# Performance work log

Hardware: AMD Instinct MI355X
Metric: run time of the kernel (lower is better)

The kernel has to match this reference:

```python
import jax, jax.numpy as jnp
import numpy as np

EPS = 1e-5

def layer_norm(x, g, b):
    m = x.mean(-1, keepdims=True)
    v = ((x - m) ** 2).mean(-1, keepdims=True)
    return (x - m) * jax.lax.rsqrt(v + EPS) * g + b

def setup_inputs() -> dict:
    key = jax.random.key(0)
    ks = jax.random.split(key, 12)
    H = 2048; E = 2048; I = 2048; N = 32
    A = (H + E) // 2  # attention hidden = 2048
    s = lambda fan: 1.0 / np.sqrt(fan)
    inp = {
        "input":   jax.random.normal(ks[0], (I,), jnp.float32),
        "hiddens": jax.random.normal(ks[1], (N, H), jnp.float32),
        "cells":   jax.random.normal(ks[2], (N, H), jnp.float32),
        "external":jax.random.normal(ks[3], (E,), jnp.float32),
        # weights (torch nn.Linear layout: [out, in]); LN enabled -> no biases on linears
        "W_ai":   jax.random.uniform(ks[4], (A, H + E), jnp.float32, -s(H+E), s(H+E)),
        "W_attn": jax.random.uniform(ks[5], (1, A), jnp.float32, -s(A), s(A)),
        "W_merge":jax.random.uniform(ks[6], (H, H), jnp.float32, -s(H), s(H)),
        "W_iou":  jax.random.uniform(ks[7], (3 * H, I + H), jnp.float32, -s(I+H), s(I+H)),
        "W_fi":   jax.random.uniform(ks[8], (H, I), jnp.float32, -s(I), s(I)),
        "W_fh":   jax.random.uniform(ks[9], (H, H), jnp.float32, -s(H), s(H)),
        "g_merge": jnp.ones((H,), jnp.float32), "b_merge": jnp.zeros((H,), jnp.float32),
        "g_f": jnp.ones((H,), jnp.float32), "b_f": jnp.zeros((H,), jnp.float32),
        "g_i": jnp.ones((H,), jnp.float32), "b_i": jnp.zeros((H,), jnp.float32),
        "g_o": jnp.ones((H,), jnp.float32), "b_o": jnp.zeros((H,), jnp.float32),
        "g_u": jnp.ones((H,), jnp.float32), "b_u": jnp.zeros((H,), jnp.float32),
        "g_c": jnp.ones((H,), jnp.float32), "b_c": jnp.zeros((H,), jnp.float32),
    }
    return inp

def reference(input, hiddens, cells, external,
              W_ai, W_attn, W_merge, W_iou, W_fi, W_fh,
              g_merge, b_merge, g_f, b_f, g_i, b_i, g_o, b_o, g_u, b_u, g_c, b_c):
    N, H = hiddens.shape
    # forget-gate preactivations: [H] + [N,H] -> [N,H]
    f_lin = input @ W_fi.T + hiddens @ W_fh.T
    # attentive merge over children
    ext = jnp.broadcast_to(external, (N, external.shape[0]))
    ai = jnp.tanh(jnp.concatenate([hiddens, ext], axis=1) @ W_ai.T)       # [N, (H+E)//2]
    attn = jax.nn.softmax(ai @ W_attn.T, axis=0)                          # [N, 1]
    merged = (hiddens * attn).sum(0)                                      # [H]
    merge_hidden = jnp.tanh(layer_norm(merged @ W_merge.T, g_merge, b_merge))
    # i/o/u gates from [input ; merged_hidden]
    iou = jnp.concatenate([input, merge_hidden]) @ W_iou.T                # [3H]
    i_l, o_l, u_l = jnp.split(iou, 3)
    f = jax.nn.sigmoid(layer_norm(f_lin, g_f, b_f))                       # [N,H]
    i = jax.nn.sigmoid(layer_norm(i_l, g_i, b_i))
    o = jax.nn.sigmoid(layer_norm(o_l, g_o, b_o))
    u = jnp.tanh(layer_norm(u_l, g_u, b_u))                               # dropout=0 -> identity
    new_cell = layer_norm(i * u + (f * cells).sum(0), g_c, b_c)           # [H]
    new_h = o * jnp.tanh(new_cell)
    return new_h, new_cell
```

## Files before the change

### kernel.cpp

```cpp
#include <hip/hip_runtime.h>
#include <hip/hip_bf16.h>

typedef __bf16 bf16_t;
typedef __attribute__((ext_vector_type(8))) __bf16 bf16x8;
typedef __attribute__((ext_vector_type(4))) float f32x4;

#define EPSF 1e-5f

__global__ __launch_bounds__(256, 3) void k1_streams(
    const float* __restrict__ hiddens, const float* __restrict__ external,
    const float* __restrict__ input,
    const float* __restrict__ W_ai, const float* __restrict__ W_fh,
    const float* __restrict__ W_fi, const float* __restrict__ W_iou,
    const float* __restrict__ W_attn,
    float* __restrict__ lp, float* __restrict__ fh_out,
    float* __restrict__ fi_out, float* __restrict__ iou_out)
{
    __shared__ float red[4][2][16][16];
    __shared__ float ejs[4][16];

    int b    = blockIdx.x;
    int tid  = threadIdx.x;
    int wave = tid >> 6;
    int lane = tid & 63;

    if (b < 256) {
        bool is_ai = (b < 128);
        int  jt    = is_ai ? b : b - 128;
        int  l15   = lane & 15;
        int  quad  = lane >> 4;
        int  k0    = wave * 512;
        int  wstride = is_ai ? 4096 : 2048;
        const float* W = is_ai ? W_ai : W_fh;

        const float* a0p = hiddens + (size_t)l15 * 2048 + quad * 8 + k0;
        const float* a1p = hiddens + (size_t)(16 + l15) * 2048 + quad * 8 + k0;
        const float* bp  = W + (size_t)(jt * 16 + l15) * wstride + quad * 8 + k0;

        f32x4 acc0 = {0.f, 0.f, 0.f, 0.f};
        f32x4 acc1 = {0.f, 0.f, 0.f, 0.f};
        float ejacc = 0.f;

        if (is_ai) {
            const float* ep = bp + 2048;
            const float* xp = external + quad * 8 + k0;
            #pragma unroll 2
            for (int k = 0; k < 512; k += 32) {
                float4 p0 = *(const float4*)(a0p + k);
                float4 p1 = *(const float4*)(a0p + k + 4);
                float4 q0 = *(const float4*)(a1p + k);
                float4 q1 = *(const float4*)(a1p + k + 4);
                float4 b0 = *(const float4*)(bp + k);
                float4 b1 = *(const float4*)(bp + k + 4);
                float4 e0 = *(const float4*)(ep + k);
                float4 e1 = *(const float4*)(ep + k + 4);
                float4 x0 = *(const float4*)(xp + k);
                float4 x1 = *(const float4*)(xp + k + 4);
                bf16x8 av0, av1, bv;
                av0[0]=(bf16_t)p0.x; av0[1]=(bf16_t)p0.y; av0[2]=(bf16_t)p0.z; av0[3]=(bf16_t)p0.w;
                av0[4]=(bf16_t)p1.x; av0[5]=(bf16_t)p1.y; av0[6]=(bf16_t)p1.z; av0[7]=(bf16_t)p1.w;
                av1[0]=(bf16_t)q0.x; av1[1]=(bf16_t)q0.y; av1[2]=(bf16_t)q0.z; av1[3]=(bf16_t)q0.w;
                av1[4]=(bf16_t)q1.x; av1[5]=(bf16_t)q1.y; av1[6]=(bf16_t)q1.z; av1[7]=(bf16_t)q1.w;
                bv[0]=(bf16_t)b0.x; bv[1]=(bf16_t)b0.y; bv[2]=(bf16_t)b0.z; bv[3]=(bf16_t)b0.w;
                bv[4]=(bf16_t)b1.x; bv[5]=(bf16_t)b1.y; bv[6]=(bf16_t)b1.z; bv[7]=(bf16_t)b1.w;
                acc0 = __builtin_amdgcn_mfma_f32_16x16x32_bf16(av0, bv, acc0, 0, 0, 0);
                acc1 = __builtin_amdgcn_mfma_f32_16x16x32_bf16(av1, bv, acc1, 0, 0, 0);
                ejacc += e0.x*x0.x + e0.y*x0.y + e0.z*x0.z + e0.w*x0.w
                       + e1.x*x1.x + e1.y*x1.y + e1.z*x1.z + e1.w*x1.w;
            }
            ejacc += __shfl_xor(ejacc, 16, 64);
            ejacc += __shfl_xor(ejacc, 32, 64);
            if (quad == 0) ejs[wave][l15] = ejacc;
        } else {
            #pragma unroll 2
            for (int k = 0; k < 512; k += 32) {
                float4 p0 = *(const float4*)(a0p + k);
                float4 p1 = *(const float4*)(a0p + k + 4);
                float4 q0 = *(const float4*)(a1p + k);
                float4 q1 = *(const float4*)(a1p + k + 4);
                float4 b0 = *(const float4*)(bp + k);
                float4 b1 = *(const float4*)(bp + k + 4);
                bf16x8 av0, av1, bv;
                av0[0]=(bf16_t)p0.x; av0[1]=(bf16_t)p0.y; av0[2]=(bf16_t)p0.z; av0[3]=(bf16_t)p0.w;
                av0[4]=(bf16_t)p1.x; av0[5]=(bf16_t)p1.y; av0[6]=(bf16_t)p1.z; av0[7]=(bf16_t)p1.w;
                av1[0]=(bf16_t)q0.x; av1[1]=(bf16_t)q0.y; av1[2]=(bf16_t)q0.z; av1[3]=(bf16_t)q0.w;
                av1[4]=(bf16_t)q1.x; av1[5]=(bf16_t)q1.y; av1[6]=(bf16_t)q1.z; av1[7]=(bf16_t)q1.w;
                bv[0]=(bf16_t)b0.x; bv[1]=(bf16_t)b0.y; bv[2]=(bf16_t)b0.z; bv[3]=(bf16_t)b0.w;
                bv[4]=(bf16_t)b1.x; bv[5]=(bf16_t)b1.y; bv[6]=(bf16_t)b1.z; bv[7]=(bf16_t)b1.w;
                acc0 = __builtin_amdgcn_mfma_f32_16x16x32_bf16(av0, bv, acc0, 0, 0, 0);
                acc1 = __builtin_amdgcn_mfma_f32_16x16x32_bf16(av1, bv, acc1, 0, 0, 0);
            }
        }

        #pragma unroll
        for (int r = 0; r < 4; ++r) {
            red[wave][0][quad * 4 + r][l15] = acc0[r];
            red[wave][1][quad * 4 + r][l15] = acc1[r];
        }
        __syncthreads();

        int row = tid >> 4, col = tid & 15;
        #pragma unroll
        for (int nt = 0; nt < 2; ++nt) {
            float s = red[0][nt][row][col] + red[1][nt][row][col]
                    + red[2][nt][row][col] + red[3][nt][row][col];
            if (is_ai) {
                float ej = ejs[0][col] + ejs[1][col] + ejs[2][col] + ejs[3][col];
                float lg = tanhf(s + ej) * W_attn[jt * 16 + col];
                lg += __shfl_xor(lg, 1, 64);
                lg += __shfl_xor(lg, 2, 64);
                lg += __shfl_xor(lg, 4, 64);
                lg += __shfl_xor(lg, 8, 64);
                if (col == 0) lp[jt * 32 + nt * 16 + row] = lg;
            } else {
                fh_out[(size_t)(nt * 16 + row) * 2048 + jt * 16 + col] = s;
            }
        }
    } else {
        const float4* in4 = (const float4*)input;
        float4 xr[8];
        #pragma unroll
        for (int k = 0; k < 8; ++k) xr[k] = in4[lane + 64 * k];

        int r0 = (b - 256) * 16 + wave * 4;
        #pragma unroll
        for (int p = 0; p < 2; ++p) {
            int ra = r0 + p * 2;
            int rb = ra + 1;
            const float4* wa = (ra < 2048)
                ? (const float4*)(W_fi + (size_t)ra * 2048)
                : (const float4*)(W_iou + (size_t)(ra - 2048) * 4096);
            const float4* wb = (rb < 2048)
                ? (const float4*)(W_fi + (size_t)rb * 2048)
                : (const float4*)(W_iou + (size_t)(rb - 2048) * 4096);
            float4 A[8], B[8];
            #pragma unroll
            for (int k = 0; k < 8; ++k) { A[k] = wa[lane + 64 * k]; B[k] = wb[lane + 64 * k]; }
            float accA = 0.f, accB = 0.f;
            #pragma unroll
            for (int k = 0; k < 8; ++k) {
                accA += A[k].x*xr[k].x + A[k].y*xr[k].y + A[k].z*xr[k].z + A[k].w*xr[k].w;
                accB += B[k].x*xr[k].x + B[k].y*xr[k].y + B[k].z*xr[k].z + B[k].w*xr[k].w;
            }
            #pragma unroll
            for (int off = 32; off; off >>= 1) {
                accA += __shfl_down(accA, off, 64);
                accB += __shfl_down(accB, off, 64);
            }
            if (lane == 0) {
                if (ra < 2048) fi_out[ra] = accA; else iou_out[ra - 2048] = accA;
                if (rb < 2048) fi_out[rb] = accB; else iou_out[rb - 2048] = accB;
            }
        }
    }
}

__global__ __launch_bounds__(256) void k2_mid(
    const float* __restrict__ fi, const float* __restrict__ fh,
    const float* __restrict__ lp, const float* __restrict__ hiddens,
    float* __restrict__ frs, float* __restrict__ merged)
{
    __shared__ float s1[256], s2[256];
    int b = blockIdx.x, t = threadIdx.x;

    if (b < 32) {
        int n = b;
        float sum = 0.f, sq = 0.f;
        #pragma unroll
        for (int i = 0; i < 8; ++i) {
            int h = t * 8 + i;
            float v = fi[h] + fh[n * 2048 + h];
            sum += v; sq += v * v;
        }
        s1[t] = sum; s2[t] = sq;
        __syncthreads();
        for (int off = 128; off; off >>= 1) {
            if (t < off) { s1[t] += s1[t + off]; s2[t] += s2[t + off]; }
            __syncthreads();
        }
        if (t == 0) {
            const float inv = 1.f / 2048.f;
            float mean = s1[0] * inv;
            frs[n * 2]     = mean;
            frs[n * 2 + 1] = rsqrtf(s2[0] * inv - mean * mean + EPSF);
        }
    } else {
        __shared__ float lred[32][8];
        __shared__ float attnw[32];
        int n = t >> 3, sl = t & 7;
        float p = 0.f;
        #pragma unroll
        for (int m = 0; m < 16; ++m) p += lp[(sl * 16 + m) * 32 + n];
        lred[n][sl] = p;
        __syncthreads();
        if (sl == 0) {
            float lg = 0.f;
            #pragma unroll
            for (int m = 0; m < 8; ++m) lg += lred[n][m];
            lred[n][0] = lg;
        }
        __syncthreads();
        if (t < 32) {
            float mx = -1e30f;
            for (int m = 0; m < 32; ++m) mx = fmaxf(mx, lred[m][0]);
            float ssum = 0.f;
            for (int m = 0; m < 32; ++m) ssum += expf(lred[m][0] - mx);
            attnw[t] = expf(lred[t][0] - mx) / ssum;
        }
        __syncthreads();
        int h = (b - 32) * 256 + t;
        float acc = 0.f;
        #pragma unroll 8
        for (int n2 = 0; n2 < 32; ++n2) acc += attnw[n2] * hiddens[n2 * 2048 + h];
        merged[h] = acc;
    }
}

__global__ __launch_bounds__(256) void k3_mid(
    const float* __restrict__ W_merge, const float* __restrict__ merged,
    const float* __restrict__ fi, const float* __restrict__ fh,
    const float* __restrict__ frs, const float* __restrict__ gf,
    const float* __restrict__ bf_, const float* __restrict__ cells,
    float* __restrict__ mm, float* __restrict__ fc)
{
    int b = blockIdx.x, t = threadIdx.x;
    int wave = t >> 6, lane = t & 63;
    if (b < 256) {
        const float4* xp = (const float4*)merged;
        float4 xr[8];
        #pragma unroll
        for (int k = 0; k < 8; ++k) xr[k] = xp[lane + 64 * k];

        int ra = b * 8 + wave * 2;
        int rb = ra + 1;
        const float4* wa = (const float4*)(W_merge + (size_t)ra * 2048);
        const float4* wb = (const float4*)(W_merge + (size_t)rb * 2048);
        float4 A[8], B[8];
        #pragma unroll
        for (int k = 0; k < 8; ++k) { A[k] = wa[lane + 64 * k]; B[k] = wb[lane + 64 * k]; }
        float accA = 0.f, accB = 0.f;
        #pragma unroll
        for (int k = 0; k < 8; ++k) {
            accA += A[k].x*xr[k].x + A[k].y*xr[k].y + A[k].z*xr[k].z + A[k].w*xr[k].w;
            accB += B[k].x*xr[k].x + B[k].y*xr[k].y + B[k].z*xr[k].z + B[k].w*xr[k].w;
        }
        #pragma unroll
        for (int off = 32; off; off >>= 1) {
            accA += __shfl_down(accA, off, 64);
            accB += __shfl_down(accB, off, 64);
        }
        if (lane == 0) { mm[ra] = accA; mm[rb] = accB; }
    } else {
        int h = (b - 256) * 256 + t;
        float g = gf[h], bb = bf_[h], f_i = fi[h];
        float acc = 0.f;
        #pragma unroll 8
        for (int n = 0; n < 32; ++n) {
            float v = (f_i + fh[n * 2048 + h] - frs[n * 2]) * frs[n * 2 + 1] * g + bb;
            float f = 1.f / (1.f + expf(-v));
            acc += f * cells[n * 2048 + h];
        }
        fc[h] = acc;
    }
}

__global__ __launch_bounds__(256, 3) void k4_mh(
    const float* __restrict__ W_iou, const float* __restrict__ mm,
    const float* __restrict__ g_merge, const float* __restrict__ b_merge,
    float* __restrict__ iou)
{
    __shared__ float mh_lds[2048];
    __shared__ float pr[4][2];
    int b = blockIdx.x, t = threadIdx.x;
    int wave = t >> 6, lane = t & 63;

    const float4* mm4 = (const float4*)mm;
    const float4* g4  = (const float4*)g_merge;
    const float4* b4  = (const float4*)b_merge;

    float4 m0 = mm4[t * 2], m1 = mm4[t * 2 + 1];
    float sum = m0.x + m0.y + m0.z + m0.w + m1.x + m1.y + m1.z + m1.w;
    float sq  = m0.x*m0.x + m0.y*m0.y + m0.z*m0.z + m0.w*m0.w
              + m1.x*m1.x + m1.y*m1.y + m1.z*m1.z + m1.w*m1.w;
    #pragma unroll
    for (int off = 1; off < 64; off <<= 1) {
        sum += __shfl_xor(sum, off, 64);
        sq  += __shfl_xor(sq,  off, 64);
    }
    if (lane == 0) { pr[wave][0] = sum; pr[wave][1] = sq; }
    __syncthreads();
    sum = pr[0][0] + pr[1][0] + pr[2][0] + pr[3][0];
    sq  = pr[0][1] + pr[1][1] + pr[2][1] + pr[3][1];
    const float inv = 1.f / 2048.f;
    float mean = sum * inv;
    float r = rsqrtf(sq * inv - mean * mean + EPSF);

    float4 g0 = g4[t * 2], g1 = g4[t * 2 + 1];
    float4 c0 = b4[t * 2], c1 = b4[t * 2 + 1];
    float4 h0, h1;
    h0.x = tanhf((m0.x - mean) * r * g0.x + c0.x);
    h0.y = tanhf((m0.y - mean) * r * g0.y + c0.y);
    h0.z = tanhf((m0.z - mean) * r * g0.z + c0.z);
    h0.w = tanhf((m0.w - mean) * r * g0.w + c0.w);
    h1.x = tanhf((m1.x - mean) * r * g1.x + c1.x);
    h1.y = tanhf((m1.y - mean) * r * g1.y + c1.y);
    h1.z = tanhf((m1.z - mean) * r * g1.z + c1.z);
    h1.w = tanhf((m1.w - mean) * r * g1.w + c1.w);
    ((float4*)mh_lds)[t * 2]     = h0;
    ((float4*)mh_lds)[t * 2 + 1] = h1;
    __syncthreads();

    float4 xr[8];
    #pragma unroll
    for (int k = 0; k < 8; ++k) xr[k] = ((const float4*)mh_lds)[lane + 64 * k];

    int ra = b * 8 + wave * 2;
    int rb = ra + 1;
    const float4* wa = (const float4*)(W_iou + (size_t)ra * 4096 + 2048);
    const float4* wb = (const float4*)(W_iou + (size_t)rb * 4096 + 2048);
    float4 A[8], B[8];
    #pragma unroll
    for (int k = 0; k < 8; ++k) { A[k] = wa[lane + 64 * k]; B[k] = wb[lane + 64 * k]; }
    float accA = 0.f, accB = 0.f;
    #pragma unroll
    for (int k = 0; k < 8; ++k) {
        accA += A[k].x*xr[k].x + A[k].y*xr[k].y + A[k].z*xr[k].z + A[k].w*xr[k].w;
        accB += B[k].x*xr[k].x + B[k].y*xr[k].y + B[k].z*xr[k].z + B[k].w*xr[k].w;
    }
    #pragma unroll
    for (int off = 32; off; off >>= 1) {
        accA += __shfl_down(accA, off, 64);
        accB += __shfl_down(accB, off, 64);
    }
    if (lane == 0) { iou[ra] += accA; iou[rb] += accB; }
}

__global__ __launch_bounds__(256) void k5_tail(
    const float* __restrict__ iou, const float* __restrict__ fc,
    const float* __restrict__ gi, const float* __restrict__ bi,
    const float* __restrict__ go, const float* __restrict__ bo,
    const float* __restrict__ gu, const float* __restrict__ bu,
    const float* __restrict__ gc, const float* __restrict__ bc,
    float* __restrict__ out)
{
    __shared__ float sA[6][256];
    int t = threadIdx.x;
    float vi[8], vo[8], vu[8];
    float si = 0, qi = 0, so = 0, qo = 0, su = 0, qu = 0;
    #pragma unroll
    for (int i = 0; i < 8; ++i) {
        int h = t * 8 + i;
        vi[i] = iou[h]; vo[i] = iou[2048 + h]; vu[i] = iou[4096 + h];
        si += vi[i]; qi += vi[i] * vi[i];
        so += vo[i]; qo += vo[i] * vo[i];
        su += vu[i]; qu += vu[i] * vu[i];
    }
    sA[0][t] = si; sA[1][t] = qi; sA[2][t] = so;
    sA[3][t] = qo; sA[4][t] = su; sA[5][t] = qu;
    __syncthreads();
    for (int off = 128; off; off >>= 1) {
        if (t < off) {
            #pragma unroll
            for (int c = 0; c < 6; ++c) sA[c][t] += sA[c][t + off];
        }
        __syncthreads();
    }
    const float inv = 1.f / 2048.f;
    float mi = sA[0][0] * inv, ri = rsqrtf(sA[1][0] * inv - mi * mi + EPSF);
    float mo = sA[2][0] * inv, ro = rsqrtf(sA[3][0] * inv - mo * mo + EPSF);
    float mu = sA[4][0] * inv, ru = rsqrtf(sA[5][0] * inv - mu * mu + EPSF);
    __syncthreads();

    float o_[8], v_[8];
    float sv = 0, qv = 0;
    #pragma unroll
    for (int i = 0; i < 8; ++i) {
        int h = t * 8 + i;
        float ivl = 1.f / (1.f + expf(-((vi[i] - mi) * ri * gi[h] + bi[h])));
        o_[i]     = 1.f / (1.f + expf(-((vo[i] - mo) * ro * go[h] + bo[h])));
        float uvl = tanhf((vu[i] - mu) * ru * gu[h] + bu[h]);
        v_[i] = ivl * uvl + fc[h];
        sv += v_[i]; qv += v_[i] * v_[i];
    }
    sA[0][t] = sv; sA[1][t] = qv;
    __syncthreads();
    for (int off = 128; off; off >>= 1) {
        if (t < off) { sA[0][t] += sA[0][t + off]; sA[1][t] += sA[1][t + off]; }
        __syncthreads();
    }
    float mc = sA[0][0] * inv, rc = rsqrtf(sA[1][0] * inv - mc * mc + EPSF);
    #pragma unroll
    for (int i = 0; i < 8; ++i) {
        int h = t * 8 + i;
        float nc = (v_[i] - mc) * rc * gc[h] + bc[h];
        float nh = o_[i] * tanhf(nc);
        out[h]        = nh;
        out[2048 + h] = nc;
    }
}

extern "C" void kernel_launch(void* const* d_in, const int* in_sizes, int n_in,
                              void* d_out, int out_size, void* d_ws, size_t ws_size,
                              hipStream_t stream)
{
    const float* input    = (const float*)d_in[0];
    const float* hiddens  = (const float*)d_in[1];
    const float* cells    = (const float*)d_in[2];
    const float* external = (const float*)d_in[3];
    const float* W_ai     = (const float*)d_in[4];
    const float* W_attn   = (const float*)d_in[5];
    const float* W_merge  = (const float*)d_in[6];
    const float* W_iou    = (const float*)d_in[7];
    const float* W_fi     = (const float*)d_in[8];
    const float* W_fh     = (const float*)d_in[9];
    const float* g_merge  = (const float*)d_in[10];
    const float* b_merge  = (const float*)d_in[11];
    const float* g_f      = (const float*)d_in[12];
    const float* b_f      = (const float*)d_in[13];
    const float* g_i      = (const float*)d_in[14];
    const float* b_i      = (const float*)d_in[15];
    const float* g_o      = (const float*)d_in[16];
    const float* b_o      = (const float*)d_in[17];
    const float* g_u      = (const float*)d_in[18];
    const float* b_u      = (const float*)d_in[19];
    const float* g_c      = (const float*)d_in[20];
    const float* b_c      = (const float*)d_in[21];

    float* ws = (float*)d_ws;
    float* ws_fh     = ws;
    float* ws_fi     = ws + 65536;
    float* ws_lp     = ws + 67584;
    float* ws_frs    = ws + 71680;
    float* ws_merged = ws + 71744;
    float* ws_mm     = ws + 73792;
    float* ws_fc     = ws + 75840;
    float* ws_iou    = ws + 77888;
    float* out = (float*)d_out;

    k1_streams<<<768, 256, 0, stream>>>(hiddens, external, input,
                                        W_ai, W_fh, W_fi, W_iou, W_attn,
                                        ws_lp, ws_fh, ws_fi, ws_iou);
    k2_mid<<<40, 256, 0, stream>>>(ws_fi, ws_fh, ws_lp, hiddens,
                                   ws_frs, ws_merged);
    k3_mid<<<264, 256, 0, stream>>>(W_merge, ws_merged, ws_fi, ws_fh,
                                    ws_frs, g_f, b_f, cells, ws_mm, ws_fc);
    k4_mh<<<768, 256, 0, stream>>>(W_iou, ws_mm, g_merge, b_merge, ws_iou);
    k5_tail<<<1, 256, 0, stream>>>(ws_iou, ws_fc, g_i, b_i, g_o, b_o,
                                   g_u, b_u, g_c, b_c, out);
}
```

Baseline: 278.5 us.

## Move input half of W_iou GEMV from k1 into k4 full-row pass

The input-side half of the W_iou matvec moves out of the first streaming kernel into the merge-hidden kernel, so k4 reads full 4096-wide W_iou rows once and writes iou directly instead of read-modify-write. k1 shrinks to 512 blocks (W_fi only), and k4 uses 256 blocks with 6 rows per wave and double-buffered register row loads. This shortens k1 but puts more weight streaming after the serial dependency chain (k2/k3), where it can no longer overlap with other independent work. Register pressure rises sharply in k4 (launch bounds set to 1 block/CU).

```diff
diff --git a/kernel.cpp b/kernel.cpp
--- a/kernel.cpp
+++ b/kernel.cpp
@@ -7,14 +7,13 @@
 
 #define EPSF 1e-5f
 
-__global__ __launch_bounds__(256, 3) void k1_streams(
+__global__ __launch_bounds__(256, 2) void k1_streams(
     const float* __restrict__ hiddens, const float* __restrict__ external,
     const float* __restrict__ input,
     const float* __restrict__ W_ai, const float* __restrict__ W_fh,
-    const float* __restrict__ W_fi, const float* __restrict__ W_iou,
-    const float* __restrict__ W_attn,
+    const float* __restrict__ W_fi, const float* __restrict__ W_attn,
     float* __restrict__ lp, float* __restrict__ fh_out,
-    float* __restrict__ fi_out, float* __restrict__ iou_out)
+    float* __restrict__ fi_out)
 {
     __shared__ float red[4][2][16][16];
     __shared__ float ejs[4][16];
@@ -122,36 +121,25 @@
         #pragma unroll
         for (int k = 0; k < 8; ++k) xr[k] = in4[lane + 64 * k];
 
-        int r0 = (b - 256) * 16 + wave * 4;
-        #pragma unroll
-        for (int p = 0; p < 2; ++p) {
-            int ra = r0 + p * 2;
-            int rb = ra + 1;
-            const float4* wa = (ra < 2048)
-                ? (const float4*)(W_fi + (size_t)ra * 2048)
-                : (const float4*)(W_iou + (size_t)(ra - 2048) * 4096);
-            const float4* wb = (rb < 2048)
-                ? (const float4*)(W_fi + (size_t)rb * 2048)
-                : (const float4*)(W_iou + (size_t)(rb - 2048) * 4096);
-            float4 A[8], B[8];
-            #pragma unroll
-            for (int k = 0; k < 8; ++k) { A[k] = wa[lane + 64 * k]; B[k] = wb[lane + 64 * k]; }
-            float accA = 0.f, accB = 0.f;
-            #pragma unroll
-            for (int k = 0; k < 8; ++k) {
-                accA += A[k].x*xr[k].x + A[k].y*xr[k].y + A[k].z*xr[k].z + A[k].w*xr[k].w;
-                accB += B[k].x*xr[k].x + B[k].y*xr[k].y + B[k].z*xr[k].z + B[k].w*xr[k].w;
-            }
-            #pragma unroll
-            for (int off = 32; off; off >>= 1) {
-                accA += __shfl_down(accA, off, 64);
-                accB += __shfl_down(accB, off, 64);
-            }
-            if (lane == 0) {
-                if (ra < 2048) fi_out[ra] = accA; else iou_out[ra - 2048] = accA;
-                if (rb < 2048) fi_out[rb] = accB; else iou_out[rb - 2048] = accB;
-            }
-        }
+        int ra = (b - 256) * 8 + wave * 2;
+        int rb = ra + 1;
+        const float4* wa = (const float4*)(W_fi + (size_t)ra * 2048);
+        const float4* wb = (const float4*)(W_fi + (size_t)rb * 2048);
+        float4 A[8], B[8];
+        #pragma unroll
+        for (int k = 0; k < 8; ++k) { A[k] = wa[lane + 64 * k]; B[k] = wb[lane + 64 * k]; }
+        float accA = 0.f, accB = 0.f;
+        #pragma unroll
+        for (int k = 0; k < 8; ++k) {
+            accA += A[k].x*xr[k].x + A[k].y*xr[k].y + A[k].z*xr[k].z + A[k].w*xr[k].w;
+            accB += B[k].x*xr[k].x + B[k].y*xr[k].y + B[k].z*xr[k].z + B[k].w*xr[k].w;
+        }
+        #pragma unroll
+        for (int off = 32; off; off >>= 1) {
+            accA += __shfl_down(accA, off, 64);
+            accB += __shfl_down(accB, off, 64);
+        }
+        if (lane == 0) { fi_out[ra] = accA; fi_out[rb] = accB; }
     }
 }
 
@@ -264,8 +252,9 @@
     }
 }
 
-__global__ __launch_bounds__(256, 3) void k4_mh(
+__global__ __launch_bounds__(256, 1) void k4_iou(
     const float* __restrict__ W_iou, const float* __restrict__ mm,
+    const float* __restrict__ input,
     const float* __restrict__ g_merge, const float* __restrict__ b_merge,
     float* __restrict__ iou)
 {
@@ -310,29 +299,49 @@
     ((float4*)mh_lds)[t * 2 + 1] = h1;
     __syncthreads();
 
-    float4 xr[8];
-    #pragma unroll
-    for (int k = 0; k < 8; ++k) xr[k] = ((const float4*)mh_lds)[lane + 64 * k];
-
-    int ra = b * 8 + wave * 2;
-    int rb = ra + 1;
-    const float4* wa = (const float4*)(W_iou + (size_t)ra * 4096 + 2048);
-    const float4* wb = (const float4*)(W_iou + (size_t)rb * 4096 + 2048);
-    float4 A[8], B[8];
-    #pragma unroll
-    for (int k = 0; k < 8; ++k) { A[k] = wa[lane + 64 * k]; B[k] = wb[lane + 64 * k]; }
-    float accA = 0.f, accB = 0.f;
-    #pragma unroll
-    for (int k = 0; k < 8; ++k) {
-        accA += A[k].x*xr[k].x + A[k].y*xr[k].y + A[k].z*xr[k].z + A[k].w*xr[k].w;
-        accB += B[k].x*xr[k].x + B[k].y*xr[k].y + B[k].z*xr[k].z + B[k].w*xr[k].w;
-    }
-    #pragma unroll
-    for (int off = 32; off; off >>= 1) {
-        accA += __shfl_down(accA, off, 64);
-        accB += __shfl_down(accB, off, 64);
-    }
-    if (lane == 0) { iou[ra] += accA; iou[rb] += accB; }
+    float4 xr[16];
+    const float4* in4 = (const float4*)input;
+    #pragma unroll
+    for (int k = 0; k < 8; ++k) xr[k] = in4[lane + 64 * k];
+    #pragma unroll
+    for (int k = 0; k < 8; ++k) xr[8 + k] = ((const float4*)mh_lds)[lane + 64 * k];
+
+    int r0 = b * 24 + wave * 6;
+    float4 A[16], B[16];
+
+    #define LDROW(dst, ri) do {                                            \
+        const float4* wp_ = (const float4*)(W_iou + (size_t)(ri) * 4096);  \
+        _Pragma("unroll")                                                  \
+        for (int k_ = 0; k_ < 16; ++k_) dst[k_] = wp_[lane + 64 * k_];     \
+    } while (0)
+
+    #define REDROW(src, ri) do {                                           \
+        float acc_ = 0.f;                                                  \
+        _Pragma("unroll")                                                  \
+        for (int k_ = 0; k_ < 16; ++k_)                                    \
+            acc_ += src[k_].x*xr[k_].x + src[k_].y*xr[k_].y                \
+                  + src[k_].z*xr[k_].z + src[k_].w*xr[k_].w;               \
+        _Pragma("unroll")                                                  \
+        for (int off_ = 32; off_; off_ >>= 1)                              \
+            acc_ += __shfl_down(acc_, off_, 64);                           \
+        if (lane == 0) iou[ri] = acc_;                                     \
+    } while (0)
+
+    LDROW(A, r0 + 0);
+    LDROW(B, r0 + 1);
+    REDROW(A, r0 + 0);
+    LDROW(A, r0 + 2);
+    REDROW(B, r0 + 1);
+    LDROW(B, r0 + 3);
+    REDROW(A, r0 + 2);
+    LDROW(A, r0 + 4);
+    REDROW(B, r0 + 3);
+    LDROW(B, r0 + 5);
+    REDROW(A, r0 + 4);
+    REDROW(B, r0 + 5);
+
+    #undef LDROW
+    #undef REDROW
 }
 
 __global__ __launch_bounds__(256) void k5_tail(
@@ -437,14 +446,15 @@
     float* ws_iou    = ws + 77888;
     float* out = (float*)d_out;
 
-    k1_streams<<<768, 256, 0, stream>>>(hiddens, external, input,
-                                        W_ai, W_fh, W_fi, W_iou, W_attn,
-                                        ws_lp, ws_fh, ws_fi, ws_iou);
+    k1_streams<<<512, 256, 0, stream>>>(hiddens, external, input,
+                                        W_ai, W_fh, W_fi, W_attn,
+                                        ws_lp, ws_fh, ws_fi);
     k2_mid<<<40, 256, 0, stream>>>(ws_fi, ws_fh, ws_lp, hiddens,
                                    ws_frs, ws_merged);
     k3_mid<<<264, 256, 0, stream>>>(W_merge, ws_merged, ws_fi, ws_fh,
                                     ws_frs, g_f, b_f, cells, ws_mm, ws_fc);
-    k4_mh<<<768, 256, 0, stream>>>(W_iou, ws_mm, g_merge, b_merge, ws_iou);
+    k4_iou<<<256, 256, 0, stream>>>(W_iou, ws_mm, input, g_merge, b_merge,
+                                    ws_iou);
     k5_tail<<<1, 256, 0, stream>>>(ws_iou, ws_fc, g_i, b_i, g_o, b_o,
                                    g_u, b_u, g_c, b_c, out);
 }
```

After: 282.1 us. About the same (+1.3%).
